# Kernel tuning notes

Measured on AMD Instinct MI355X. Metric: run time of the kernel, lower is better.

## Reference

```python
import jax, jax.numpy as jnp
import numpy as np

T = 4          # number of atom types (H, C, N, O)
D = 384        # aev_length
H0, H1, H2 = 160, 128, 96
B, A = 2048, 64
ALPHA = 0.1    # CELU alpha


def celu(x, alpha=ALPHA):
    return jnp.where(x > 0, x, alpha * jnp.expm1(x / alpha))


def setup_inputs() -> dict:
    key = jax.random.key(0)
    ks = jax.random.split(key, 6)
    species = jax.random.randint(ks[0], (B, A), 0, T, dtype=jnp.int32)
    aev = jax.random.normal(ks[1], (B, A, D), dtype=jnp.float32)

    def w(k, shape, fan_in):
        return (jax.random.normal(k, shape, dtype=jnp.float32) / np.sqrt(fan_in)).astype(jnp.float32)

    # stacked per-type weights: leading axis T
    W0 = w(ks[2], (T, D, H0), D);   b0 = jnp.zeros((T, H0), jnp.float32)
    W1 = w(ks[3], (T, H0, H1), H0); b1 = jnp.zeros((T, H1), jnp.float32)
    W2 = w(ks[4], (T, H1, H2), H1); b2 = jnp.zeros((T, H2), jnp.float32)
    W3 = w(ks[5], (T, H2, 1), H2);  b3 = jnp.zeros((T, 1), jnp.float32)
    return dict(species=species, aev=aev,
                W0=W0, b0=b0, W1=W1, b1=b1, W2=W2, b2=b2, W3=W3, b3=b3)


def reference(species, aev, W0, b0, W1, b1, W2, b2, W3, b3):
    # species: [B, A] int32 in [0, T); aev: [B, A, D]
    sp = species.reshape(-1)            # [N]
    x = aev.reshape(-1, D)              # [N, D]
    # Run every type's MLP over all atoms (T is small), then select per atom.
    h = celu(jnp.einsum('nd,tdh->tnh', x, W0) + b0[:, None, :])   # [T, N, H0]
    h = celu(jnp.einsum('tnh,thk->tnk', h, W1) + b1[:, None, :])  # [T, N, H1]
    h = celu(jnp.einsum('tnk,tkm->tnm', h, W2) + b2[:, None, :])  # [T, N, H2]
    o = jnp.einsum('tnm,tmo->tno', h, W3) + b3[:, None, :]        # [T, N, 1]
    o = o[..., 0]                                                  # [T, N]
    per_atom = jnp.take_along_axis(o, sp[None, :], axis=0)[0]     # [N]
    energies = per_atom.reshape(species.shape).sum(axis=1)        # [B]
    return species, energies
```

## Files before the change

### kernel.cpp

```cpp
#include <hip/hip_runtime.h>
#include <hip/hip_bf16.h>

#define DD 384
#define NB 2048
#define NA 64
#define NN (NB*NA)

using bhalf8 = __attribute__((ext_vector_type(8))) __bf16;
using f32x4  = __attribute__((ext_vector_type(4))) float;
typedef unsigned short u16;
typedef unsigned char u8;

#define AS1 __attribute__((address_space(1)))
#define AS3 __attribute__((address_space(3)))

__device__ __forceinline__ void gl_lds16(const void* g, void* l) {
  __builtin_amdgcn_global_load_lds((const AS1 void*)g, (AS3 void*)l, 16, 0, 0);
}

__device__ __forceinline__ u16 f2b(float f) {
  __hip_bfloat16 h = __float2bfloat16(f);
  union { __hip_bfloat16 h; u16 u; } c; c.h = h; return c.u;
}
__device__ __forceinline__ float b2f(u16 u) {
  union { unsigned int i; float f; } c; c.i = ((unsigned int)u) << 16; return c.f;
}
__device__ __forceinline__ float celu_f(float v) {
  return v > 0.f ? v : 0.1f * (__expf(v * 10.f) - 1.f);
}
__device__ __forceinline__ bhalf8 pack8(float4 a, float4 b) {
  union { u16 us[8]; bhalf8 v; } t;
  t.us[0]=f2b(a.x); t.us[1]=f2b(a.y); t.us[2]=f2b(a.z); t.us[3]=f2b(a.w);
  t.us[4]=f2b(b.x); t.us[5]=f2b(b.y); t.us[6]=f2b(b.z); t.us[7]=f2b(b.w);
  return t.v;
}


__global__ void k_prep(const int* __restrict__ species, int* __restrict__ counts,
                       float* __restrict__ out_sp,
                       const float* __restrict__ W0, const float* __restrict__ W1,
                       const float* __restrict__ W2, const float* __restrict__ W3,
                       u16* __restrict__ W0img, u16* __restrict__ W1img,
                       u16* __restrict__ W2img, u16* __restrict__ W3B) {
  int tid = threadIdx.x;
  int id = blockIdx.x * 256 + tid;
  if (blockIdx.x < 512) {
    __shared__ int lcnt[4];
    if (tid < 4) lcnt[tid] = 0;
    __syncthreads();
    int s = species[id];
    out_sp[id] = (float)s;
    atomicAdd(&lcnt[s], 1);
    __syncthreads();
    if (tid < 4) atomicAdd(&counts[tid], lcnt[tid]);
  }
  if (id < 270336) {
    int t = id / 67584, r1 = id % 67584;
    int kc = r1 / 5632, r2 = r1 % 5632;
    int r = r2 >> 5, rem = r2 & 31, s = rem >> 3, e = rem & 7;
    u16 v = 0;
    if (r < 160) {
      int k = kc * 32 + (s ^ ((r >> 1) & 3)) * 8 + e;
      v = f2b(W0[t * 61440 + k * 160 + r]);
    }
    W0img[id] = v;
  } else if ((id -= 270336) < 81920) {
    int t = id / 20480, r1 = id % 20480;
    int kc = r1 / 4096, r2 = r1 % 4096;
    int r = r2 >> 5, rem = r2 & 31, s = rem >> 3, e = rem & 7;
    int k = kc * 32 + (s ^ ((r >> 1) & 3)) * 8 + e;
    W1img[id] = f2b(W1[t * 20480 + k * 128 + r]);
  } else if ((id -= 81920) < 65536) {
    int t = id / 16384, r1 = id % 16384;
    int kc = r1 / 4096, r2 = r1 % 4096;
    int r = r2 >> 5, rem = r2 & 31, s = rem >> 3, e = rem & 7;
    u16 v = 0;
    if (r < 96) {
      int k = kc * 32 + (s ^ ((r >> 1) & 3)) * 8 + e;
      v = f2b(W2[t * 12288 + k * 96 + r]);
    }
    W2img[id] = v;
  } else if ((id -= 65536) < 384) {
    W3B[id] = f2b(W3[id]);
  }
}

__global__ void k_scatter(const int* __restrict__ species, const int* __restrict__ counts,
                          int* __restrict__ cursors, int* __restrict__ sorted) {
  __shared__ int lcnt[4];
  __shared__ int lbase[4];
  int tid = threadIdx.x;
  if (tid < 4) lcnt[tid] = 0;
  __syncthreads();
  int i = blockIdx.x * 256 + tid;
  int s = species[i];
  int lpos = atomicAdd(&lcnt[s], 1);
  __syncthreads();
  if (tid < 4) {
    int offs = 0;
    #pragma unroll
    for (int t = 0; t < 4; ++t) if (t < tid) offs += counts[t];
    lbase[tid] = offs + atomicAdd(&cursors[tid], lcnt[tid]);
  }
  __syncthreads();
  sorted[lbase[s] + lpos] = i;
}


__global__ __launch_bounds__(256, 3) void k_mlp(
    const float* __restrict__ aev, const int* __restrict__ sorted,
    const int* __restrict__ counts,
    const u16* __restrict__ W0img, const u16* __restrict__ W1img,
    const u16* __restrict__ W2img, const u16* __restrict__ W3B,
    const float* __restrict__ b0, const float* __restrict__ b1,
    const float* __restrict__ b2, const float* __restrict__ b3,
    float* __restrict__ atom_out)
{
  int type = blockIdx.x, tile = blockIdx.y;
  int c0 = counts[0], c1 = counts[1], c2 = counts[2], c3 = counts[3];
  int cnt = (type == 0) ? c0 : (type == 1) ? c1 : (type == 2) ? c2 : c3;
  if (tile * 64 >= cnt) return;
  int off = 0;
  if (type > 0) off += c0;
  if (type > 1) off += c1;
  if (type > 2) off += c2;

  __shared__ uint4 smem4[2752];
  u8* smem = (u8*)smem4;
  u8*  Bst = smem;
  u8*  Ast = smem + 22528;
  u16* sH0 = (u16*)(smem + 22528);
  u16* sH1 = (u16*)(smem + 22528);
  u16* sH2 = (u16*)(smem + 22528);

  int tid = threadIdx.x, lane = tid & 63, w = tid >> 6;
  int wm = w & 1, wn = w >> 1, l15 = lane & 15, lk = lane >> 4;
  int base = off + tile * 64, nvalid = min(64, cnt - tile * 64);

  float bia0[5], bia1[4], bia2[3], bia3;
  #pragma unroll
  for (int nt = 0; nt < 5; ++nt) bia0[nt] = b0[type * 160 + wn * 80 + nt * 16 + l15];
  #pragma unroll
  for (int nt = 0; nt < 4; ++nt) bia1[nt] = b1[type * 128 + wn * 64 + nt * 16 + l15];
  #pragma unroll
  for (int nt = 0; nt < 3; ++nt) bia2[nt] = b2[type * 96 + wn * 48 + nt * 16 + l15];
  bia3 = b3[type];

  int arow0 = w * 16 + (lane >> 3), arow1 = arow0 + 8;
  const float* a0 = aev + (size_t)sorted[base + min(arow0, nvalid - 1)] * DD
                    + (((lane & 7) ^ (arow0 & 7)) << 2);
  const float* a1 = aev + (size_t)sorted[base + min(arow1, nvalid - 1)] * DD
                    + (((lane & 7) ^ (arow1 & 7)) << 2);
  const u8* gB0 = (const u8*)W0img + (size_t)type * 135168 + w * 1024 + lane * 16;
  const u8* gW1 = (const u8*)W1img + (size_t)type * 40960  + w * 1024 + lane * 16;
  const u8* gW2 = (const u8*)W2img + (size_t)type * 32768  + w * 1024 + lane * 16;
  u8* dA = Ast + 2 * w * 1024;
  u8* dB = Bst + w * 1024;

#define STG_L0(KC, B_) do { \
    gl_lds16(a0 + (KC) * 32, dA + (B_) * 8192); \
    gl_lds16(a1 + (KC) * 32, dA + (B_) * 8192 + 1024); \
    gl_lds16(gB0 + (KC) * 11264,        dB + (B_) * 11264); \
    gl_lds16(gB0 + (KC) * 11264 + 4096, dB + (B_) * 11264 + 4096); \
    if (w < 3) gl_lds16(gB0 + (KC) * 11264 + 8192, dB + (B_) * 11264 + 8192); \
  } while (0)
#define STG_W(IMG, KC, B_) do { \
    gl_lds16((IMG) + (KC) * 8192,        dB + (B_) * 11264); \
    gl_lds16((IMG) + (KC) * 8192 + 4096, dB + (B_) * 11264 + 4096); \
  } while (0)

  int rA0 = wm * 32 + l15, rA1 = rA0 + 16;
  int sAa = (((2 * lk)     ^ (rA0 & 7)) << 4);
  int sAb = (((2 * lk + 1) ^ (rA0 & 7)) << 4);
  int aoff0 = rA0 * 128, aoff1 = rA1 * 128;
  int bsw = (lk ^ ((l15 >> 1) & 3)) << 4;

#define TOPW(WN) \
  asm volatile("s_waitcnt vmcnt(" #WN ")" ::: "memory"); \
  __builtin_amdgcn_sched_barrier(0); \
  __builtin_amdgcn_s_barrier(); \
  __builtin_amdgcn_sched_barrier(0);
#define TAILW() \
  asm volatile("s_waitcnt lgkmcnt(0)" ::: "memory"); \
  __builtin_amdgcn_sched_barrier(0); \
  __builtin_amdgcn_s_barrier(); \
  __builtin_amdgcn_sched_barrier(0);

  f32x4 acc0[2][5];
  #pragma unroll
  for (int mt = 0; mt < 2; ++mt)
    #pragma unroll
    for (int nt = 0; nt < 5; ++nt) acc0[mt][nt] = f32x4{0.f, 0.f, 0.f, 0.f};

  STG_L0(0, 0);
  STG_L0(1, 1);

#define PHA(KC, WN, STG_) \
  TOPW(WN) \
  { const u8* bA = Ast + ((KC) & 1) * 8192; \
    const u8* bB = Bst + ((KC) & 1) * 11264; \
    bhalf8 af0 = pack8(*(const float4*)(bA + aoff0 + sAa), *(const float4*)(bA + aoff0 + sAb)); \
    bhalf8 af1 = pack8(*(const float4*)(bA + aoff1 + sAa), *(const float4*)(bA + aoff1 + sAb)); \
    bhalf8 bf[5]; \
    _Pragma("unroll") \
    for (int nt = 0; nt < 5; ++nt) \
      bf[nt] = *(const bhalf8*)(bB + ((wn * 80 + nt * 16 + l15) << 6) + bsw); \
    _Pragma("unroll") \
    for (int nt = 0; nt < 5; ++nt) { \
      acc0[0][nt] = __builtin_amdgcn_mfma_f32_16x16x32_bf16(af0, bf[nt], acc0[0][nt], 0, 0, 0); \
      acc0[1][nt] = __builtin_amdgcn_mfma_f32_16x16x32_bf16(af1, bf[nt], acc0[1][nt], 0, 0, 0); \
    } } \
  TAILW() \
  STG_;

  PHA(0, 4, STG_L0(2, 0))  PHA(1, 4, STG_L0(3, 1))  PHA(2, 4, STG_L0(4, 0))
  PHA(3, 4, STG_L0(5, 1))  PHA(4, 4, STG_L0(6, 0))  PHA(5, 4, STG_L0(7, 1))
  PHA(6, 4, STG_L0(8, 0))  PHA(7, 4, STG_L0(9, 1))  PHA(8, 4, STG_L0(10, 0))
  PHA(9, 4, STG_L0(11, 1)) PHA(10, 4, STG_W(gW1, 0, 0)) PHA(11, 2, STG_W(gW1, 1, 1))
#undef PHA

  #pragma unroll
  for (int mt = 0; mt < 2; ++mt)
    #pragma unroll
    for (int nt = 0; nt < 5; ++nt) {
      int col = wn * 80 + nt * 16 + l15;
      #pragma unroll
      for (int i = 0; i < 4; ++i) {
        int row = wm * 32 + mt * 16 + lk * 4 + i;
        sH0[row * 168 + col] = f2b(celu_f(acc0[mt][nt][i] + bia0[nt]));
      }
    }
  asm volatile("s_waitcnt lgkmcnt(0)" ::: "memory");
  __builtin_amdgcn_sched_barrier(0);

  f32x4 acc1[2][4];
  #pragma unroll
  for (int mt = 0; mt < 2; ++mt)
    #pragma unroll
    for (int nt = 0; nt < 4; ++nt) acc1[mt][nt] = f32x4{0.f, 0.f, 0.f, 0.f};

#define PHB(KC, WN, STG_) \
  TOPW(WN) \
  { const u8* bB = Bst + ((KC) & 1) * 11264; \
    bhalf8 af0 = *(const bhalf8*)&sH0[(wm * 32 + l15) * 168 + (KC) * 32 + lk * 8]; \
    bhalf8 af1 = *(const bhalf8*)&sH0[(wm * 32 + 16 + l15) * 168 + (KC) * 32 + lk * 8]; \
    bhalf8 bf[4]; \
    _Pragma("unroll") \
    for (int nt = 0; nt < 4; ++nt) \
      bf[nt] = *(const bhalf8*)(bB + ((wn * 64 + nt * 16 + l15) << 6) + bsw); \
    _Pragma("unroll") \
    for (int nt = 0; nt < 4; ++nt) { \
      acc1[0][nt] = __builtin_amdgcn_mfma_f32_16x16x32_bf16(af0, bf[nt], acc1[0][nt], 0, 0, 0); \
      acc1[1][nt] = __builtin_amdgcn_mfma_f32_16x16x32_bf16(af1, bf[nt], acc1[1][nt], 0, 0, 0); \
    } } \
  TAILW() \
  STG_;

  PHB(0, 2, STG_W(gW1, 2, 0)) PHB(1, 2, STG_W(gW1, 3, 1)) PHB(2, 2, STG_W(gW1, 4, 0))
  PHB(3, 2, STG_W(gW2, 0, 1)) PHB(4, 2, STG_W(gW2, 1, 0))
#undef PHB

  #pragma unroll
  for (int mt = 0; mt < 2; ++mt)
    #pragma unroll
    for (int nt = 0; nt < 4; ++nt) {
      int col = wn * 64 + nt * 16 + l15;
      #pragma unroll
      for (int i = 0; i < 4; ++i) {
        int row = wm * 32 + mt * 16 + lk * 4 + i;
        sH1[row * 136 + col] = f2b(celu_f(acc1[mt][nt][i] + bia1[nt]));
      }
    }
  asm volatile("s_waitcnt lgkmcnt(0)" ::: "memory");
  __builtin_amdgcn_sched_barrier(0);

  f32x4 acc2[2][3];
  #pragma unroll
  for (int mt = 0; mt < 2; ++mt)
    #pragma unroll
    for (int nt = 0; nt < 3; ++nt) acc2[mt][nt] = f32x4{0.f, 0.f, 0.f, 0.f};

#define PHC(KC, WN, STG_) \
  TOPW(WN) \
  { const u8* bB = Bst + (((KC) + 1) & 1) * 11264; \
    bhalf8 af0 = *(const bhalf8*)&sH1[(wm * 32 + l15) * 136 + (KC) * 32 + lk * 8]; \
    bhalf8 af1 = *(const bhalf8*)&sH1[(wm * 32 + 16 + l15) * 136 + (KC) * 32 + lk * 8]; \
    bhalf8 bf[3]; \
    _Pragma("unroll") \
    for (int nt = 0; nt < 3; ++nt) \
      bf[nt] = *(const bhalf8*)(bB + ((wn * 48 + nt * 16 + l15) << 6) + bsw); \
    _Pragma("unroll") \
    for (int nt = 0; nt < 3; ++nt) { \
      acc2[0][nt] = __builtin_amdgcn_mfma_f32_16x16x32_bf16(af0, bf[nt], acc2[0][nt], 0, 0, 0); \
      acc2[1][nt] = __builtin_amdgcn_mfma_f32_16x16x32_bf16(af1, bf[nt], acc2[1][nt], 0, 0, 0); \
    } } \
  TAILW() \
  STG_;

  PHC(0, 2, STG_W(gW2, 2, 1)) PHC(1, 2, STG_W(gW2, 3, 0)) PHC(2, 2, ) PHC(3, 0, )
#undef PHC
#undef STG_L0
#undef STG_W

  #pragma unroll
  for (int mt = 0; mt < 2; ++mt)
    #pragma unroll
    for (int nt = 0; nt < 3; ++nt) {
      int col = wn * 48 + nt * 16 + l15;
      #pragma unroll
      for (int i = 0; i < 4; ++i) {
        int row = wm * 32 + mt * 16 + lk * 4 + i;
        sH2[row * 104 + col] = f2b(celu_f(acc2[mt][nt][i] + bia2[nt]));
      }
    }
  asm volatile("s_waitcnt lgkmcnt(0)" ::: "memory");
  __builtin_amdgcn_sched_barrier(0);
  __builtin_amdgcn_s_barrier();
  __builtin_amdgcn_sched_barrier(0);

  {
    int atom = tid >> 2;
    int q = tid & 3;
    const u16* w3 = W3B + type * 96 + q * 24;
    const u16* hrow = sH2 + atom * 104 + q * 24;
    float s = 0.f;
    #pragma unroll
    for (int i = 0; i < 3; ++i) {
      union { bhalf8 v; u16 u[8]; } hu, wu;
      hu.v = *(const bhalf8*)&hrow[i * 8];
      wu.v = *(const bhalf8*)&w3[i * 8];
      #pragma unroll
      for (int j = 0; j < 8; ++j)
        s += b2f(hu.u[j]) * b2f(wu.u[j]);
    }
    s += __shfl_xor(s, 1);
    s += __shfl_xor(s, 2);
    if (q == 0 && atom < nvalid)
      atom_out[sorted[base + atom]] = s + bia3;
  }
}

__global__ void k_reduce(const float* __restrict__ atom_out, float* __restrict__ out_e) {
  int mol = blockIdx.x;
  int lane = threadIdx.x;
  float v = atom_out[mol * 64 + lane];
  #pragma unroll
  for (int m = 32; m >= 1; m >>= 1) v += __shfl_xor(v, m);
  if (lane == 0) out_e[mol] = v;
}


extern "C" void kernel_launch(void* const* d_in, const int* in_sizes, int n_in,
                              void* d_out, int out_size, void* d_ws, size_t ws_size,
                              hipStream_t stream) {
  const int*   species = (const int*)d_in[0];
  const float* aev = (const float*)d_in[1];
  const float* W0 = (const float*)d_in[2];
  const float* b0 = (const float*)d_in[3];
  const float* W1 = (const float*)d_in[4];
  const float* b1 = (const float*)d_in[5];
  const float* W2 = (const float*)d_in[6];
  const float* b2 = (const float*)d_in[7];
  const float* W3 = (const float*)d_in[8];
  const float* b3 = (const float*)d_in[9];
  float* out = (float*)d_out;

  unsigned char* ws = (unsigned char*)d_ws;
  int* counts = (int*)(ws + 0);
  int* sorted = (int*)(ws + 64);
  float* atom_out = (float*)(ws + 524352);
  u16* W0img = (u16*)(ws + 1048640);
  u16* W1img = (u16*)(ws + 1589312);
  u16* W2img = (u16*)(ws + 1753152);
  u16* W3B   = (u16*)(ws + 1884224);

  hipMemsetAsync(counts, 0, 48, stream);
  k_prep<<<1634, 256, 0, stream>>>(species, counts, out,
        W0, W1, W2, W3, W0img, W1img, W2img, W3B);
  k_scatter<<<NN / 256, 256, 0, stream>>>(species, counts, counts + 8, sorted);
  k_mlp<<<dim3(4, 2048), 256, 0, stream>>>(aev, sorted, counts,
        W0img, W1img, W2img, W3B, b0, b1, b2, b3, atom_out);
  k_reduce<<<NB, 64, 0, stream>>>(atom_out, out + NN);
}
```

Baseline: 84.31 us.

## Double MLP tile to 128 atoms with 512-thread blocks and fuse energy reduction

Each block now processes 128 atoms of one species using 8 waves: four split the rows and two split the columns, so every staged weight tile is shared by twice as many atoms. The staging macros and wait counts are rewritten to match, and shared memory grows to 64KB. The separate per-molecule reduction kernel is removed. Per-atom energies are atomically added into a zeroed output instead, which saves a launch and a global round trip but adds float atomic contention and makes the summation order nondeterministic.

```diff
diff --git a/kernel.cpp b/kernel.cpp
--- a/kernel.cpp
+++ b/kernel.cpp
@@ -107,25 +107,25 @@
 }
 
 
-__global__ __launch_bounds__(256, 3) void k_mlp(
+__global__ __launch_bounds__(512, 4) void k_mlp(
     const float* __restrict__ aev, const int* __restrict__ sorted,
     const int* __restrict__ counts,
     const u16* __restrict__ W0img, const u16* __restrict__ W1img,
     const u16* __restrict__ W2img, const u16* __restrict__ W3B,
     const float* __restrict__ b0, const float* __restrict__ b1,
     const float* __restrict__ b2, const float* __restrict__ b3,
-    float* __restrict__ atom_out)
+    float* __restrict__ outE)
 {
   int type = blockIdx.x, tile = blockIdx.y;
   int c0 = counts[0], c1 = counts[1], c2 = counts[2], c3 = counts[3];
   int cnt = (type == 0) ? c0 : (type == 1) ? c1 : (type == 2) ? c2 : c3;
-  if (tile * 64 >= cnt) return;
+  if (tile * 128 >= cnt) return;
   int off = 0;
   if (type > 0) off += c0;
   if (type > 1) off += c1;
   if (type > 2) off += c2;
 
-  __shared__ uint4 smem4[2752];
+  __shared__ uint4 smem4[4096];
   u8* smem = (u8*)smem4;
   u8*  Bst = smem;
   u8*  Ast = smem + 22528;
@@ -134,16 +134,17 @@
   u16* sH2 = (u16*)(smem + 22528);
 
   int tid = threadIdx.x, lane = tid & 63, w = tid >> 6;
-  int wm = w & 1, wn = w >> 1, l15 = lane & 15, lk = lane >> 4;
-  int base = off + tile * 64, nvalid = min(64, cnt - tile * 64);
+  int wm2 = w & 3, wn2 = w >> 2, l15 = lane & 15, lk = lane >> 4;
+  int base = off + tile * 128, nvalid = min(128, cnt - tile * 128);
+  int wu = __builtin_amdgcn_readfirstlane(w);
 
   float bia0[5], bia1[4], bia2[3], bia3;
   #pragma unroll
-  for (int nt = 0; nt < 5; ++nt) bia0[nt] = b0[type * 160 + wn * 80 + nt * 16 + l15];
-  #pragma unroll
-  for (int nt = 0; nt < 4; ++nt) bia1[nt] = b1[type * 128 + wn * 64 + nt * 16 + l15];
-  #pragma unroll
-  for (int nt = 0; nt < 3; ++nt) bia2[nt] = b2[type * 96 + wn * 48 + nt * 16 + l15];
+  for (int nt = 0; nt < 5; ++nt) bia0[nt] = b0[type * 160 + wn2 * 80 + nt * 16 + l15];
+  #pragma unroll
+  for (int nt = 0; nt < 4; ++nt) bia1[nt] = b1[type * 128 + wn2 * 64 + nt * 16 + l15];
+  #pragma unroll
+  for (int nt = 0; nt < 3; ++nt) bia2[nt] = b2[type * 96 + wn2 * 48 + nt * 16 + l15];
   bia3 = b3[type];
 
   int arow0 = w * 16 + (lane >> 3), arow1 = arow0 + 8;
@@ -154,37 +155,39 @@
   const u8* gB0 = (const u8*)W0img + (size_t)type * 135168 + w * 1024 + lane * 16;
   const u8* gW1 = (const u8*)W1img + (size_t)type * 40960  + w * 1024 + lane * 16;
   const u8* gW2 = (const u8*)W2img + (size_t)type * 32768  + w * 1024 + lane * 16;
-  u8* dA = Ast + 2 * w * 1024;
+  u8* dA = Ast + w * 2048;
   u8* dB = Bst + w * 1024;
 
 #define STG_L0(KC, B_) do { \
-    gl_lds16(a0 + (KC) * 32, dA + (B_) * 8192); \
-    gl_lds16(a1 + (KC) * 32, dA + (B_) * 8192 + 1024); \
-    gl_lds16(gB0 + (KC) * 11264,        dB + (B_) * 11264); \
-    gl_lds16(gB0 + (KC) * 11264 + 4096, dB + (B_) * 11264 + 4096); \
-    if (w < 3) gl_lds16(gB0 + (KC) * 11264 + 8192, dB + (B_) * 11264 + 8192); \
+    gl_lds16(a0 + (KC) * 32, dA + (B_) * 16384); \
+    gl_lds16(a1 + (KC) * 32, dA + (B_) * 16384 + 1024); \
+    gl_lds16(gB0 + (KC) * 11264, dB + (B_) * 11264); \
+    if (wu < 3) gl_lds16(gB0 + (KC) * 11264 + 8192, dB + (B_) * 11264 + 8192); \
   } while (0)
-#define STG_W(IMG, KC, B_) do { \
-    gl_lds16((IMG) + (KC) * 8192,        dB + (B_) * 11264); \
-    gl_lds16((IMG) + (KC) * 8192 + 4096, dB + (B_) * 11264 + 4096); \
-  } while (0)
-
-  int rA0 = wm * 32 + l15, rA1 = rA0 + 16;
-  int sAa = (((2 * lk)     ^ (rA0 & 7)) << 4);
-  int sAb = (((2 * lk + 1) ^ (rA0 & 7)) << 4);
-  int aoff0 = rA0 * 128, aoff1 = rA1 * 128;
+#define STG_W(IMG, KC, B_) \
+    gl_lds16((IMG) + (KC) * 8192, dB + (B_) * 11264)
+
+  int aoff0 = (wm2 * 32 + l15) * 128, aoff1 = aoff0 + 2048;
+  int sAa = (((2 * lk)     ^ (l15 & 7)) << 4);
+  int sAb = (((2 * lk + 1) ^ (l15 & 7)) << 4);
   int bsw = (lk ^ ((l15 >> 1) & 3)) << 4;
 
-#define TOPW(WN) \
+#define TOPL0() do { \
+  if (wu < 3) asm volatile("s_waitcnt vmcnt(4)" ::: "memory"); \
+  else        asm volatile("s_waitcnt vmcnt(3)" ::: "memory"); \
+  __builtin_amdgcn_sched_barrier(0); \
+  __builtin_amdgcn_s_barrier(); \
+  __builtin_amdgcn_sched_barrier(0); } while (0)
+#define TOPN(WN) do { \
   asm volatile("s_waitcnt vmcnt(" #WN ")" ::: "memory"); \
   __builtin_amdgcn_sched_barrier(0); \
   __builtin_amdgcn_s_barrier(); \
-  __builtin_amdgcn_sched_barrier(0);
-#define TAILW() \
+  __builtin_amdgcn_sched_barrier(0); } while (0)
+#define TAILW() do { \
   asm volatile("s_waitcnt lgkmcnt(0)" ::: "memory"); \
   __builtin_amdgcn_sched_barrier(0); \
   __builtin_amdgcn_s_barrier(); \
-  __builtin_amdgcn_sched_barrier(0);
+  __builtin_amdgcn_sched_barrier(0); } while (0)
 
   f32x4 acc0[2][5];
   #pragma unroll
@@ -195,38 +198,39 @@
   STG_L0(0, 0);
   STG_L0(1, 1);
 
-#define PHA(KC, WN, STG_) \
-  TOPW(WN) \
-  { const u8* bA = Ast + ((KC) & 1) * 8192; \
+#define PHA_BODY(KC) \
+  { const u8* bA = Ast + ((KC) & 1) * 16384; \
     const u8* bB = Bst + ((KC) & 1) * 11264; \
     bhalf8 af0 = pack8(*(const float4*)(bA + aoff0 + sAa), *(const float4*)(bA + aoff0 + sAb)); \
     bhalf8 af1 = pack8(*(const float4*)(bA + aoff1 + sAa), *(const float4*)(bA + aoff1 + sAb)); \
     bhalf8 bf[5]; \
     _Pragma("unroll") \
     for (int nt = 0; nt < 5; ++nt) \
-      bf[nt] = *(const bhalf8*)(bB + ((wn * 80 + nt * 16 + l15) << 6) + bsw); \
+      bf[nt] = *(const bhalf8*)(bB + ((wn2 * 80 + nt * 16 + l15) << 6) + bsw); \
     _Pragma("unroll") \
     for (int nt = 0; nt < 5; ++nt) { \
       acc0[0][nt] = __builtin_amdgcn_mfma_f32_16x16x32_bf16(af0, bf[nt], acc0[0][nt], 0, 0, 0); \
       acc0[1][nt] = __builtin_amdgcn_mfma_f32_16x16x32_bf16(af1, bf[nt], acc0[1][nt], 0, 0, 0); \
-    } } \
-  TAILW() \
-  STG_;
-
-  PHA(0, 4, STG_L0(2, 0))  PHA(1, 4, STG_L0(3, 1))  PHA(2, 4, STG_L0(4, 0))
-  PHA(3, 4, STG_L0(5, 1))  PHA(4, 4, STG_L0(6, 0))  PHA(5, 4, STG_L0(7, 1))
-  PHA(6, 4, STG_L0(8, 0))  PHA(7, 4, STG_L0(9, 1))  PHA(8, 4, STG_L0(10, 0))
-  PHA(9, 4, STG_L0(11, 1)) PHA(10, 4, STG_W(gW1, 0, 0)) PHA(11, 2, STG_W(gW1, 1, 1))
+    } }
+
+#define PHA(KC, STG_) TOPL0(); PHA_BODY(KC) TAILW(); STG_;
+
+  PHA(0, STG_L0(2, 0))  PHA(1, STG_L0(3, 1))  PHA(2, STG_L0(4, 0))
+  PHA(3, STG_L0(5, 1))  PHA(4, STG_L0(6, 0))  PHA(5, STG_L0(7, 1))
+  PHA(6, STG_L0(8, 0))  PHA(7, STG_L0(9, 1))  PHA(8, STG_L0(10, 0))
+  PHA(9, STG_L0(11, 1)) PHA(10, STG_W(gW1, 0, 0))
+  TOPN(1); PHA_BODY(11) TAILW(); STG_W(gW1, 1, 1);
 #undef PHA
+#undef PHA_BODY
 
   #pragma unroll
   for (int mt = 0; mt < 2; ++mt)
     #pragma unroll
     for (int nt = 0; nt < 5; ++nt) {
-      int col = wn * 80 + nt * 16 + l15;
+      int col = wn2 * 80 + nt * 16 + l15;
       #pragma unroll
       for (int i = 0; i < 4; ++i) {
-        int row = wm * 32 + mt * 16 + lk * 4 + i;
+        int row = wm2 * 32 + mt * 16 + lk * 4 + i;
         sH0[row * 168 + col] = f2b(celu_f(acc0[mt][nt][i] + bia0[nt]));
       }
     }
@@ -239,35 +243,35 @@
     #pragma unroll
     for (int nt = 0; nt < 4; ++nt) acc1[mt][nt] = f32x4{0.f, 0.f, 0.f, 0.f};
 
-#define PHB(KC, WN, STG_) \
-  TOPW(WN) \
+#define PHB(KC, STG_) \
+  TOPN(1); \
   { const u8* bB = Bst + ((KC) & 1) * 11264; \
-    bhalf8 af0 = *(const bhalf8*)&sH0[(wm * 32 + l15) * 168 + (KC) * 32 + lk * 8]; \
-    bhalf8 af1 = *(const bhalf8*)&sH0[(wm * 32 + 16 + l15) * 168 + (KC) * 32 + lk * 8]; \
+    bhalf8 af0 = *(const bhalf8*)&sH0[(wm2 * 32 + l15) * 168 + (KC) * 32 + lk * 8]; \
+    bhalf8 af1 = *(const bhalf8*)&sH0[(wm2 * 32 + 16 + l15) * 168 + (KC) * 32 + lk * 8]; \
     bhalf8 bf[4]; \
     _Pragma("unroll") \
     for (int nt = 0; nt < 4; ++nt) \
-      bf[nt] = *(const bhalf8*)(bB + ((wn * 64 + nt * 16 + l15) << 6) + bsw); \
+      bf[nt] = *(const bhalf8*)(bB + ((wn2 * 64 + nt * 16 + l15) << 6) + bsw); \
     _Pragma("unroll") \
     for (int nt = 0; nt < 4; ++nt) { \
       acc1[0][nt] = __builtin_amdgcn_mfma_f32_16x16x32_bf16(af0, bf[nt], acc1[0][nt], 0, 0, 0); \
       acc1[1][nt] = __builtin_amdgcn_mfma_f32_16x16x32_bf16(af1, bf[nt], acc1[1][nt], 0, 0, 0); \
     } } \
-  TAILW() \
+  TAILW(); \
   STG_;
 
-  PHB(0, 2, STG_W(gW1, 2, 0)) PHB(1, 2, STG_W(gW1, 3, 1)) PHB(2, 2, STG_W(gW1, 4, 0))
-  PHB(3, 2, STG_W(gW2, 0, 1)) PHB(4, 2, STG_W(gW2, 1, 0))
+  PHB(0, STG_W(gW1, 2, 0)) PHB(1, STG_W(gW1, 3, 1)) PHB(2, STG_W(gW1, 4, 0))
+  PHB(3, STG_W(gW2, 0, 1)) PHB(4, STG_W(gW2, 1, 0))
 #undef PHB
 
   #pragma unroll
   for (int mt = 0; mt < 2; ++mt)
     #pragma unroll
     for (int nt = 0; nt < 4; ++nt) {
-      int col = wn * 64 + nt * 16 + l15;
+      int col = wn2 * 64 + nt * 16 + l15;
       #pragma unroll
       for (int i = 0; i < 4; ++i) {
-        int row = wm * 32 + mt * 16 + lk * 4 + i;
+        int row = wm2 * 32 + mt * 16 + lk * 4 + i;
         sH1[row * 136 + col] = f2b(celu_f(acc1[mt][nt][i] + bia1[nt]));
       }
     }
@@ -281,23 +285,23 @@
     for (int nt = 0; nt < 3; ++nt) acc2[mt][nt] = f32x4{0.f, 0.f, 0.f, 0.f};
 
 #define PHC(KC, WN, STG_) \
-  TOPW(WN) \
+  TOPN(WN); \
   { const u8* bB = Bst + (((KC) + 1) & 1) * 11264; \
-    bhalf8 af0 = *(const bhalf8*)&sH1[(wm * 32 + l15) * 136 + (KC) * 32 + lk * 8]; \
-    bhalf8 af1 = *(const bhalf8*)&sH1[(wm * 32 + 16 + l15) * 136 + (KC) * 32 + lk * 8]; \
+    bhalf8 af0 = *(const bhalf8*)&sH1[(wm2 * 32 + l15) * 136 + (KC) * 32 + lk * 8]; \
+    bhalf8 af1 = *(const bhalf8*)&sH1[(wm2 * 32 + 16 + l15) * 136 + (KC) * 32 + lk * 8]; \
     bhalf8 bf[3]; \
     _Pragma("unroll") \
     for (int nt = 0; nt < 3; ++nt) \
-      bf[nt] = *(const bhalf8*)(bB + ((wn * 48 + nt * 16 + l15) << 6) + bsw); \
+      bf[nt] = *(const bhalf8*)(bB + ((wn2 * 48 + nt * 16 + l15) << 6) + bsw); \
     _Pragma("unroll") \
     for (int nt = 0; nt < 3; ++nt) { \
       acc2[0][nt] = __builtin_amdgcn_mfma_f32_16x16x32_bf16(af0, bf[nt], acc2[0][nt], 0, 0, 0); \
       acc2[1][nt] = __builtin_amdgcn_mfma_f32_16x16x32_bf16(af1, bf[nt], acc2[1][nt], 0, 0, 0); \
     } } \
-  TAILW() \
+  TAILW(); \
   STG_;
 
-  PHC(0, 2, STG_W(gW2, 2, 1)) PHC(1, 2, STG_W(gW2, 3, 0)) PHC(2, 2, ) PHC(3, 0, )
+  PHC(0, 1, STG_W(gW2, 2, 1)) PHC(1, 1, STG_W(gW2, 3, 0)) PHC(2, 1, ) PHC(3, 0, )
 #undef PHC
 #undef STG_L0
 #undef STG_W
@@ -306,10 +310,10 @@
   for (int mt = 0; mt < 2; ++mt)
     #pragma unroll
     for (int nt = 0; nt < 3; ++nt) {
-      int col = wn * 48 + nt * 16 + l15;
+      int col = wn2 * 48 + nt * 16 + l15;
       #pragma unroll
       for (int i = 0; i < 4; ++i) {
-        int row = wm * 32 + mt * 16 + lk * 4 + i;
+        int row = wm2 * 32 + mt * 16 + lk * 4 + i;
         sH2[row * 104 + col] = f2b(celu_f(acc2[mt][nt][i] + bia2[nt]));
       }
     }
@@ -326,27 +330,20 @@
     float s = 0.f;
     #pragma unroll
     for (int i = 0; i < 3; ++i) {
-      union { bhalf8 v; u16 u[8]; } hu, wu;
+      union { bhalf8 v; u16 u[8]; } hu, wu2;
       hu.v = *(const bhalf8*)&hrow[i * 8];
-      wu.v = *(const bhalf8*)&w3[i * 8];
+      wu2.v = *(const bhalf8*)&w3[i * 8];
       #pragma unroll
       for (int j = 0; j < 8; ++j)
-        s += b2f(hu.u[j]) * b2f(wu.u[j]);
+        s += b2f(hu.u[j]) * b2f(wu2.u[j]);
     }
     s += __shfl_xor(s, 1);
     s += __shfl_xor(s, 2);
-    if (q == 0 && atom < nvalid)
-      atom_out[sorted[base + atom]] = s + bia3;
+    if (q == 0 && atom < nvalid) {
+      int ai = sorted[base + atom];
+      atomicAdd(&outE[ai >> 6], s + bia3);
+    }
   }
-}
-
-__global__ void k_reduce(const float* __restrict__ atom_out, float* __restrict__ out_e) {
-  int mol = blockIdx.x;
-  int lane = threadIdx.x;
-  float v = atom_out[mol * 64 + lane];
-  #pragma unroll
-  for (int m = 32; m >= 1; m >>= 1) v += __shfl_xor(v, m);
-  if (lane == 0) out_e[mol] = v;
 }
 
 
@@ -368,17 +365,16 @@
   unsigned char* ws = (unsigned char*)d_ws;
   int* counts = (int*)(ws + 0);
   int* sorted = (int*)(ws + 64);
-  float* atom_out = (float*)(ws + 524352);
   u16* W0img = (u16*)(ws + 1048640);
   u16* W1img = (u16*)(ws + 1589312);
   u16* W2img = (u16*)(ws + 1753152);
   u16* W3B   = (u16*)(ws + 1884224);
 
   hipMemsetAsync(counts, 0, 48, stream);
+  hipMemsetAsync(out + NN, 0, NB * 4, stream);
   k_prep<<<1634, 256, 0, stream>>>(species, counts, out,
         W0, W1, W2, W3, W0img, W1img, W2img, W3B);
   k_scatter<<<NN / 256, 256, 0, stream>>>(species, counts, counts + 8, sorted);
-  k_mlp<<<dim3(4, 2048), 256, 0, stream>>>(aev, sorted, counts,
-        W0img, W1img, W2img, W3B, b0, b1, b2, b3, atom_out);
-  k_reduce<<<NB, 64, 0, stream>>>(atom_out, out + NN);
-}
+  k_mlp<<<dim3(4, 1024), 512, 0, stream>>>(aev, sorted, counts,
+        W0img, W1img, W2img, W3B, b0, b1, b2, b3, out + NN);
+}
```

Result: slower. 112.1 us (+33.0%).
